# Performance work log

Measured on AMD Instinct MI355X. Metric: run time of the kernel, lower is better.

Reference implementation:

```python
import jax, jax.numpy as jnp
import numpy as np

K = 32  # neighbors per query point


def _gather_points(x, idx):
    # x: [B, N, D], idx: [B, M, k] -> [B, M, k, D]
    B, M, k = idx.shape
    D = x.shape[-1]
    flat = jnp.take_along_axis(x, idx.reshape(B, M * k, 1), axis=1)
    return flat.reshape(B, M, k, D)


def setup_inputs() -> dict:
    key = jax.random.key(0)
    k1, k2, k3, k4, k5 = jax.random.split(key, 5)
    B, N, M, Cin = 16, 4096, 1024, 64
    pos = jax.random.normal(k1, (B, N, 3), dtype=jnp.float32)
    features = jax.random.normal(k2, (B, N, Cin), dtype=jnp.float32)
    idx = jax.random.randint(k3, (B, M), 0, N, dtype=jnp.int64)
    # 1x1 conv2d MLP params: (Cin+3) -> 64 -> 128 (use_xyz adds 3 channels)
    W1 = jax.random.normal(k4, (Cin + 3, 64), dtype=jnp.float32) * (1.0 / np.sqrt(Cin + 3))
    b1 = jnp.zeros((64,), dtype=jnp.float32)
    W2 = jax.random.normal(k5, (64, 128), dtype=jnp.float32) * (1.0 / np.sqrt(64))
    b2 = jnp.zeros((128,), dtype=jnp.float32)
    return {"pos": pos, "features": features, "W1": W1, "b1": b1,
            "W2": W2, "b2": b2, "idx": idx}


def reference(pos, features, W1, b1, W2, b2, idx):
    # pos: [B,N,3], features: [B,N,C], idx: [B,M] query-point indices
    pos_q = jnp.take_along_axis(pos, idx[..., None], axis=1)  # [B,M,3]
    # squared-distance knn: [B,M,N]
    d2 = (jnp.sum(pos_q ** 2, -1, keepdims=True)
          + jnp.sum(pos ** 2, -1)[:, None, :]
          - 2.0 * jnp.einsum("bmd,bnd->bmn", pos_q, pos))
    _, nn_idx = jax.lax.top_k(-d2, K)  # [B,M,K] nearest neighbors
    grouped_pos = _gather_points(pos, nn_idx)          # [B,M,K,3]
    grouped_feat = _gather_points(features, nn_idx)    # [B,M,K,C]
    rel = grouped_pos - pos_q[:, :, None, :]           # recenter groups
    x = jnp.concatenate([rel, grouped_feat], axis=-1)  # [B,M,K,C+3] (use_xyz)
    # 1x1 conv2d MLP == per-point linear + ReLU on channel dim
    h = jax.nn.relu(jnp.einsum("bmkc,cd->bmkd", x, W1) + b1)
    h = jax.nn.relu(jnp.einsum("bmkc,cd->bmkd", h, W2) + b2)
    out = jnp.max(h, axis=-2)  # max over K neighbors -> [B,M,128]
    return (pos_q, out)
```

## Files before the change

### kernel.cpp

```cpp
#include <hip/hip_runtime.h>

#define NPTS  4096
#define MQ    1024
#define BATCH 16
#define KNN   32
#define CIN   64
#define H1D   64
#define H2D   128

typedef _Float16 half8 __attribute__((ext_vector_type(8)));
typedef float    floatx4 __attribute__((ext_vector_type(4)));

#define WS_NN_BYTES ((size_t)BATCH * MQ * KNN * 4)
#define W1F_HALVES  (3 * 4 * 64 * 8)
#define W2F_HALVES  (2 * 8 * 64 * 8)
#define WS_P4_OFF   (WS_NN_BYTES + (W1F_HALVES + W2F_HALVES) * 2)

__global__ __launch_bounds__(256) void wprep_kernel(
    const float* __restrict__ W1, const float* __restrict__ W2,
    const float* __restrict__ pos,
    _Float16* __restrict__ wout, float4* __restrict__ pos4)
{
    const int gid = blockIdx.x * 256 + threadIdx.x;
    if (gid < 768) {
        const int s = gid;
        const int kc = s >> 8, nt = (s >> 6) & 3, lane = s & 63;
        const int col = lane & 15, quad = lane >> 4;
        half8 ph;
#pragma unroll
        for (int j = 0; j < 8; ++j) {
            const int k = kc * 32 + quad * 8 + j;
            ph[j] = (k < 67) ? (_Float16)W1[k * H1D + nt * 16 + col] : (_Float16)0.0f;
        }
        *(half8*)(wout + (size_t)s * 8) = ph;
    } else if (gid < 1792) {
        const int s2 = gid - 768;
        const int kc2 = s2 >> 9, nt2 = (s2 >> 6) & 7, lane = s2 & 63;
        const int col = lane & 15, quad = lane >> 4;
        half8 ph;
#pragma unroll
        for (int j = 0; j < 8; ++j) {
            const int k = kc2 * 32 + quad * 8 + j;
            ph[j] = (_Float16)W2[k * H2D + nt2 * 16 + col];
        }
        *(half8*)(wout + (size_t)W1F_HALVES + (size_t)s2 * 8) = ph;
    } else {
        const int p = gid - 1792;
        if (p < BATCH * NPTS) {
            const float px = pos[p * 3 + 0], py = pos[p * 3 + 1], pz = pos[p * 3 + 2];
            float4 v;
            v.x = px; v.y = py; v.z = pz;
            v.w = __fadd_rn(__fadd_rn(__fmul_rn(px, px), __fmul_rn(py, py)),
                            __fmul_rn(pz, pz));
            pos4[p] = v;
        }
    }
}

__global__ __launch_bounds__(256, 4) void knn_kernel(
    const float4* __restrict__ pos4, const int* __restrict__ idx,
    float* __restrict__ pos_q, int* __restrict__ nn)
{
    const int bid = blockIdx.x;
    const int b   = bid >> 10;
    const int m   = bid & (MQ - 1);
    const int t   = threadIdx.x;
    const int wv  = t >> 6, lane = t & 63;

    __shared__ unsigned int hist[2048];
    __shared__ unsigned int wsum[4];
    __shared__ unsigned int sc[8];
    __shared__ unsigned int ckey[64];
    __shared__ int          cidx[64];
    __shared__ int          outidx[KNN];

    const float4* pb4 = pos4 + (size_t)b * NPTS;
    const int qn = idx[(size_t)b * MQ + m];
    const float4 qv = pb4[qn];
    const float qq = qv.w;

#pragma unroll
    for (int j = 0; j < 8; ++j) hist[t + 256 * j] = 0u;
    __syncthreads();

    float4 p[16];
#pragma unroll
    for (int i = 0; i < 16; ++i) p[i] = pb4[i * 256 + t];

    unsigned int k[16];
#pragma unroll
    for (int i = 0; i < 16; ++i) {
        const float qp = __fadd_rn(__fadd_rn(__fmul_rn(qv.x, p[i].x), __fmul_rn(qv.y, p[i].y)),
                                   __fmul_rn(qv.z, p[i].z));
        const float d2 = __fsub_rn(__fadd_rn(qq, p[i].w), __fmul_rn(2.0f, qp));
        unsigned int u = __float_as_uint(d2);
        u = (u & 0x80000000u) ? ~u : (u | 0x80000000u);
        k[i] = u;
        atomicAdd(&hist[u >> 21], 1u);
    }
    __syncthreads();

    unsigned int prefix = 0u, rank = KNN - 1;
    int shift = 21, bcnt;
    for (int level = 0; level < 3; ++level) {
        const int nb = (level < 2) ? 11 : 10;
        const int g  = (1 << nb) >> 8;
        unsigned int cnt[8];
        unsigned int s = 0;
        for (int j = 0; j < g; ++j) { cnt[j] = hist[t * g + j]; s += cnt[j]; }
        unsigned int v = s;
#pragma unroll
        for (int off = 1; off < 64; off <<= 1) {
            const unsigned int o = __shfl_up(v, off);
            if (lane >= off) v += o;
        }
        if (lane == 63) wsum[wv] = v;
        __syncthreads();
        unsigned int woff = 0;
        for (int i = 0; i < wv; ++i) woff += wsum[i];
        const unsigned int incl = woff + v, excl = incl - s;
        if (rank >= excl && rank < incl) {
            unsigned int e = excl;
            for (int j = 0; j < g; ++j) {
                if (rank < e + cnt[j]) {
                    sc[0] = (prefix << nb) | (unsigned int)(t * g + j);
                    sc[1] = rank - e;
                    sc[2] = cnt[j];
                    break;
                }
                e += cnt[j];
            }
        }
        __syncthreads();
        prefix = sc[0];
        rank   = sc[1];
        bcnt   = (int)sc[2];
        if (level == 2 || bcnt <= 64) break;

        const int nshift = (level == 0) ? 10 : 0;
        const int nnb    = (level == 0) ? 11 : 10;
        const unsigned int nmask = (1u << nnb) - 1u;
        __syncthreads();
#pragma unroll
        for (int j = 0; j < 8; ++j) hist[t + 256 * j] = 0u;
        __syncthreads();
#pragma unroll
        for (int i = 0; i < 16; ++i) {
            const unsigned int u = k[i];
            if ((u >> (nshift + nnb)) == prefix)
                atomicAdd(&hist[(u >> nshift) & nmask], 1u);
        }
        shift = nshift;
        __syncthreads();
    }

    if (t == 0) { sc[3] = 0u; sc[4] = 0u; }
    __syncthreads();
#pragma unroll
    for (int i = 0; i < 16; ++i) {
        const unsigned int u = k[i];
        const unsigned int hp = (shift == 0) ? u : (u >> shift);
        if (hp < prefix) {
            outidx[atomicAdd(&sc[3], 1u)] = i * 256 + t;
        } else if (hp == prefix) {
            const unsigned int slot = atomicAdd(&sc[4], 1u);
            if (slot < 64u) { ckey[slot] = u; cidx[slot] = i * 256 + t; }
        }
    }
    __syncthreads();
    const int defcnt  = (int)sc[3];
    const int candcnt = min((int)sc[4], 64);

    if (wv == 0) {
        const unsigned int k_l = (lane < candcnt) ? ckey[lane] : 0xFFFFFFFFu;
        const int          i_l = (lane < candcnt) ? cidx[lane] : 0x7FFFFFFF;
        int rk = 0;
        for (int j = 0; j < candcnt; ++j) {
            const unsigned int kj = __shfl(k_l, j);
            const int          ij = __shfl(i_l, j);
            if (kj < k_l || (kj == k_l && ij < i_l)) ++rk;
        }
        if (lane < candcnt && rk <= (int)rank) outidx[defcnt + rk] = i_l;
    }
    __syncthreads();
    if (t < KNN) nn[(size_t)bid * KNN + t] = outidx[t];
    if (t == 0) {
        pos_q[(size_t)bid * 3 + 0] = qv.x;
        pos_q[(size_t)bid * 3 + 1] = qv.y;
        pos_q[(size_t)bid * 3 + 2] = qv.z;
    }
}

__global__ __launch_bounds__(256, 4) void mlp_kernel(
    const float4* __restrict__ pos4, const float* __restrict__ feat,
    const float* __restrict__ b1, const float* __restrict__ b2,
    const float* __restrict__ pos_q, const int* __restrict__ nn,
    const _Float16* __restrict__ wf, float* __restrict__ out)
{
    __shared__ _Float16 sh[4 * 3072];
    const int t = threadIdx.x;
    const int w = t >> 6, lane = t & 63;
    const int col = lane & 15, quad = lane >> 4;
    const int q = blockIdx.x * 4 + w;
    const int b = q >> 10;
    const int wbase = w * 3072;

    {
        const int r = t >> 1, h = t & 1;
        const int kk = r & 31;
        const int n = nn[(size_t)q * KNN + kk];
        const float4 pv = pos4[(size_t)b * NPTS + n];
        const float4* f4 = (const float4*)(feat + ((size_t)b * NPTS + n) * CIN);
        const int mt = kk >> 4, lrow = kk & 15;
        if (h == 0) {
            float4 ff[12];
#pragma unroll
            for (int ii = 0; ii < 12; ++ii) ff[ii] = f4[ii];
            float rel[3];
            rel[0] = pv.x - pos_q[(size_t)q * 3 + 0];
            rel[1] = pv.y - pos_q[(size_t)q * 3 + 1];
            rel[2] = pv.z - pos_q[(size_t)q * 3 + 2];
#pragma unroll
            for (int ci = 0; ci < 6; ++ci) {
                half8 ph;
#pragma unroll
                for (int jj = 0; jj < 8; ++jj) {
                    const int c = ci * 8 + jj;
                    float v;
                    if (c < 3) v = rel[c];
                    else {
                        const int fc = c - 3;
                        const float4 vv = ff[fc >> 2];
                        v = ((fc & 3) == 0) ? vv.x : ((fc & 3) == 1) ? vv.y
                          : ((fc & 3) == 2) ? vv.z : vv.w;
                    }
                    ph[jj] = (_Float16)v;
                }
                const int kc = ci >> 2, qd = ci & 3;
                *(half8*)&sh[wbase + ((kc * 2 + mt) * 64 + qd * 16 + lrow) * 8] = ph;
            }
        } else {
            float4 ff[5];
#pragma unroll
            for (int ii = 0; ii < 5; ++ii) ff[ii] = f4[11 + ii];
#pragma unroll
            for (int ci = 6; ci < 12; ++ci) {
                half8 ph;
#pragma unroll
                for (int jj = 0; jj < 8; ++jj) {
                    const int c = ci * 8 + jj;
                    float v = 0.0f;
                    if (c < 67) {
                        const int fc = c - 3;
                        const float4 vv = ff[(fc >> 2) - 11];
                        v = ((fc & 3) == 0) ? vv.x : ((fc & 3) == 1) ? vv.y
                          : ((fc & 3) == 2) ? vv.z : vv.w;
                    }
                    ph[jj] = (_Float16)v;
                }
                const int kc = ci >> 2, qd = ci & 3;
                *(half8*)&sh[wbase + ((kc * 2 + mt) * 64 + qd * 16 + lrow) * 8] = ph;
            }
        }
    }

    half8 af[3][2];
#pragma unroll
    for (int kc = 0; kc < 3; ++kc)
#pragma unroll
        for (int mt = 0; mt < 2; ++mt)
            af[kc][mt] = *(const half8*)&sh[wbase + ((kc * 2 + mt) * 64 + lane) * 8];

    half8 w1f[3][4];
#pragma unroll
    for (int kc = 0; kc < 3; ++kc)
#pragma unroll
        for (int nt = 0; nt < 4; ++nt)
            w1f[kc][nt] = *(const half8*)(wf + (size_t)((kc * 4 + nt) * 64 + lane) * 8);

#pragma unroll
    for (int nt = 0; nt < 4; ++nt) {
        const float bv = b1[nt * 16 + col];
        floatx4 acc0 = {bv, bv, bv, bv}, acc1 = acc0;
#pragma unroll
        for (int kc = 0; kc < 3; ++kc) {
            acc0 = __builtin_amdgcn_mfma_f32_16x16x32_f16(af[kc][0], w1f[kc][nt], acc0, 0, 0, 0);
            acc1 = __builtin_amdgcn_mfma_f32_16x16x32_f16(af[kc][1], w1f[kc][nt], acc1, 0, 0, 0);
        }
        const int kc2 = nt >> 1;
        const int quad2 = (((nt & 1) * 16) + col) >> 3;
        const int j2 = col & 7;
#pragma unroll
        for (int mt = 0; mt < 2; ++mt) {
            const floatx4 a = mt ? acc1 : acc0;
#pragma unroll
            for (int reg = 0; reg < 4; ++reg) {
                const int row = quad * 4 + reg;
                sh[wbase + ((kc2 * 2 + mt) * 64 + quad2 * 16 + row) * 8 + j2] =
                    (_Float16)fmaxf(a[reg], 0.0f);
            }
        }
    }

    half8 a2[2][2];
#pragma unroll
    for (int kc2 = 0; kc2 < 2; ++kc2)
#pragma unroll
        for (int mt = 0; mt < 2; ++mt)
            a2[kc2][mt] = *(const half8*)&sh[wbase + ((kc2 * 2 + mt) * 64 + lane) * 8];

    half8 w2f[2][8];
#pragma unroll
    for (int kc2 = 0; kc2 < 2; ++kc2)
#pragma unroll
        for (int nt2 = 0; nt2 < 8; ++nt2)
            w2f[kc2][nt2] = *(const half8*)(wf + (size_t)W1F_HALVES
                                            + (size_t)((kc2 * 8 + nt2) * 64 + lane) * 8);

    float* oq = out + (size_t)q * H2D;
#pragma unroll
    for (int nt2 = 0; nt2 < 8; ++nt2) {
        const float bv = b2[nt2 * 16 + col];
        floatx4 acc0 = {bv, bv, bv, bv}, acc1 = acc0;
#pragma unroll
        for (int kc2 = 0; kc2 < 2; ++kc2) {
            acc0 = __builtin_amdgcn_mfma_f32_16x16x32_f16(a2[kc2][0], w2f[kc2][nt2], acc0, 0, 0, 0);
            acc1 = __builtin_amdgcn_mfma_f32_16x16x32_f16(a2[kc2][1], w2f[kc2][nt2], acc1, 0, 0, 0);
        }
        float mm = fmaxf(fmaxf(fmaxf(acc0[0], acc0[1]), fmaxf(acc0[2], acc0[3])),
                         fmaxf(fmaxf(acc1[0], acc1[1]), fmaxf(acc1[2], acc1[3])));
        mm = fmaxf(mm, 0.0f);
        mm = fmaxf(mm, __shfl_xor(mm, 16));
        mm = fmaxf(mm, __shfl_xor(mm, 32));
        if (lane < 16) oq[nt2 * 16 + lane] = mm;
    }
}

extern "C" void kernel_launch(void* const* d_in, const int* in_sizes, int n_in,
                              void* d_out, int out_size, void* d_ws, size_t ws_size,
                              hipStream_t stream)
{
    const float* pos  = (const float*)d_in[0];
    const float* feat = (const float*)d_in[1];
    const float* W1   = (const float*)d_in[2];
    const float* b1   = (const float*)d_in[3];
    const float* W2   = (const float*)d_in[4];
    const float* b2   = (const float*)d_in[5];
    const int*   idx  = (const int*)d_in[6];

    float* pos_q = (float*)d_out;
    float* out   = (float*)d_out + (size_t)BATCH * MQ * 3;
    int*      nn = (int*)d_ws;
    _Float16* wf = (_Float16*)((char*)d_ws + WS_NN_BYTES);
    float4*   p4 = (float4*)((char*)d_ws + WS_P4_OFF);

    const int prep_threads = 1792 + BATCH * NPTS;
    wprep_kernel<<<(prep_threads + 255) / 256, 256, 0, stream>>>(W1, W2, pos, wf, p4);
    knn_kernel<<<BATCH * MQ, 256, 0, stream>>>(p4, idx, pos_q, nn);
    mlp_kernel<<<BATCH * MQ / 4, 256, 0, stream>>>(p4, feat, b1, b2,
                                                   pos_q, nn, wf, out);
}
```

Baseline: 196.7 us.

## Use data-adaptive range-normalized radix select in KNN kernel

The KNN radix selection now does a block-wide min/max reduction of the distance keys, subtracts the minimum, and builds 1024-bin histograms over only the occupied bit range. The fixed 11/11/10-bit scheme wasted most of its first-level bins on the sign and exponent bits. The aim is to cut histogram passes and shrink shared-memory histogram work, with vectorized uint4 clears and reads. The cost is an extra reduction and barrier, and a possibly different number of refinement levels.

```diff
diff --git a/kernel.cpp b/kernel.cpp
--- a/kernel.cpp
+++ b/kernel.cpp
@@ -67,7 +67,8 @@
     const int t   = threadIdx.x;
     const int wv  = t >> 6, lane = t & 63;
 
-    __shared__ unsigned int hist[2048];
+    __shared__ __align__(16) unsigned int hist[1024];
+    __shared__ unsigned int wred[8];
     __shared__ unsigned int wsum[4];
     __shared__ unsigned int sc[8];
     __shared__ unsigned int ckey[64];
@@ -79,15 +80,14 @@
     const float4 qv = pb4[qn];
     const float qq = qv.w;
 
-#pragma unroll
-    for (int j = 0; j < 8; ++j) hist[t + 256 * j] = 0u;
-    __syncthreads();
+    *(uint4*)&hist[t * 4] = make_uint4(0u, 0u, 0u, 0u);
 
     float4 p[16];
 #pragma unroll
     for (int i = 0; i < 16; ++i) p[i] = pb4[i * 256 + t];
 
     unsigned int k[16];
+    unsigned int lmin = 0xFFFFFFFFu, lmax = 0u;
 #pragma unroll
     for (int i = 0; i < 16; ++i) {
         const float qp = __fadd_rn(__fadd_rn(__fmul_rn(qv.x, p[i].x), __fmul_rn(qv.y, p[i].y)),
@@ -96,19 +96,39 @@
         unsigned int u = __float_as_uint(d2);
         u = (u & 0x80000000u) ? ~u : (u | 0x80000000u);
         k[i] = u;
-        atomicAdd(&hist[u >> 21], 1u);
-    }
+        lmin = min(lmin, u);
+        lmax = max(lmax, u);
+    }
+#pragma unroll
+    for (int off = 32; off; off >>= 1) {
+        lmin = min(lmin, (unsigned int)__shfl_xor(lmin, off));
+        lmax = max(lmax, (unsigned int)__shfl_xor(lmax, off));
+    }
+    if (lane == 0) { wred[wv] = lmin; wred[4 + wv] = lmax; }
+    __syncthreads();
+    const unsigned int umin = min(min(wred[0], wred[1]), min(wred[2], wred[3]));
+    const unsigned int umax = max(max(wred[4], wred[5]), max(wred[6], wred[7]));
+    const unsigned int rng  = umax - umin;
+#pragma unroll
+    for (int i = 0; i < 16; ++i) k[i] -= umin;
+
+    int sCur;
+    {
+        const int bits = (rng == 0u) ? 0 : (32 - __clz(rng));
+        sCur = (bits > 10) ? (bits - 10) : 0;
+    }
+
+#pragma unroll
+    for (int i = 0; i < 16; ++i) atomicAdd(&hist[k[i] >> sCur], 1u);
     __syncthreads();
 
     unsigned int prefix = 0u, rank = KNN - 1;
-    int shift = 21, bcnt;
-    for (int level = 0; level < 3; ++level) {
-        const int nb = (level < 2) ? 11 : 10;
-        const int g  = (1 << nb) >> 8;
-        unsigned int cnt[8];
-        unsigned int s = 0;
-        for (int j = 0; j < g; ++j) { cnt[j] = hist[t * g + j]; s += cnt[j]; }
-        unsigned int v = s;
+    int bcnt = 0, nb = 0;
+    bool first = true;
+    for (;;) {
+        const uint4 c4 = *(const uint4*)&hist[t * 4];
+        const unsigned int ssum = c4.x + c4.y + c4.z + c4.w;
+        unsigned int v = ssum;
 #pragma unroll
         for (int off = 1; off < 64; off <<= 1) {
             const unsigned int o = __shfl_up(v, off);
@@ -118,12 +138,13 @@
         __syncthreads();
         unsigned int woff = 0;
         for (int i = 0; i < wv; ++i) woff += wsum[i];
-        const unsigned int incl = woff + v, excl = incl - s;
+        const unsigned int incl = woff + v, excl = incl - ssum;
         if (rank >= excl && rank < incl) {
+            const unsigned int cnt[4] = {c4.x, c4.y, c4.z, c4.w};
             unsigned int e = excl;
-            for (int j = 0; j < g; ++j) {
+            for (int j = 0; j < 4; ++j) {
                 if (rank < e + cnt[j]) {
-                    sc[0] = (prefix << nb) | (unsigned int)(t * g + j);
+                    sc[0] = (unsigned int)(t * 4 + j);
                     sc[1] = rank - e;
                     sc[2] = cnt[j];
                     break;
@@ -132,39 +153,38 @@
             }
         }
         __syncthreads();
-        prefix = sc[0];
-        rank   = sc[1];
-        bcnt   = (int)sc[2];
-        if (level == 2 || bcnt <= 64) break;
-
-        const int nshift = (level == 0) ? 10 : 0;
-        const int nnb    = (level == 0) ? 11 : 10;
-        const unsigned int nmask = (1u << nnb) - 1u;
-        __syncthreads();
-#pragma unroll
-        for (int j = 0; j < 8; ++j) hist[t + 256 * j] = 0u;
-        __syncthreads();
+        const unsigned int bin = sc[0];
+        rank = sc[1];
+        bcnt = (int)sc[2];
+        prefix = first ? bin : ((prefix << nb) | bin);
+        first = false;
+        if (bcnt <= 64 || sCur == 0) break;
+
+        const int sNext = (sCur > 10) ? (sCur - 10) : 0;
+        nb = sCur - sNext;
+        __syncthreads();
+        *(uint4*)&hist[t * 4] = make_uint4(0u, 0u, 0u, 0u);
+        __syncthreads();
+        const unsigned int mask = (1u << nb) - 1u;
 #pragma unroll
         for (int i = 0; i < 16; ++i) {
-            const unsigned int u = k[i];
-            if ((u >> (nshift + nnb)) == prefix)
-                atomicAdd(&hist[(u >> nshift) & nmask], 1u);
-        }
-        shift = nshift;
-        __syncthreads();
+            if ((k[i] >> sCur) == prefix)
+                atomicAdd(&hist[(k[i] >> sNext) & mask], 1u);
+        }
+        __syncthreads();
+        sCur = sNext;
     }
 
     if (t == 0) { sc[3] = 0u; sc[4] = 0u; }
     __syncthreads();
 #pragma unroll
     for (int i = 0; i < 16; ++i) {
-        const unsigned int u = k[i];
-        const unsigned int hp = (shift == 0) ? u : (u >> shift);
+        const unsigned int hp = k[i] >> sCur;
         if (hp < prefix) {
             outidx[atomicAdd(&sc[3], 1u)] = i * 256 + t;
         } else if (hp == prefix) {
             const unsigned int slot = atomicAdd(&sc[4], 1u);
-            if (slot < 64u) { ckey[slot] = u; cidx[slot] = i * 256 + t; }
+            if (slot < 64u) { ckey[slot] = k[i]; cidx[slot] = i * 256 + t; }
         }
     }
     __syncthreads();
```

New measurement: 190.4 us. 3.2% less time.

## Replace radix-histogram kNN select with group-min threshold filter and rank sort

Applied to the files above, without the earlier changes.

Replaces the multi-level radix histogram selection in the kNN kernel with a threshold computed as the 32nd smallest of 64 per-group minima, which is an upper bound on the 32nd-nearest distance. Points at or below the threshold are compacted into shared memory and ranked by an O(n^2) pairwise count, with a slow 32-round argmin fallback if more than 512 candidates survive. This removes the histogram clears, shared atomics and repeated scans, at the cost of a candidate count that depends on the data and possible extra work in the fallback path.

```diff
diff --git a/kernel.cpp b/kernel.cpp
--- a/kernel.cpp
+++ b/kernel.cpp
@@ -61,33 +61,31 @@
     const float4* __restrict__ pos4, const int* __restrict__ idx,
     float* __restrict__ pos_q, int* __restrict__ nn)
 {
+    const int KCAP = 512;
     const int bid = blockIdx.x;
     const int b   = bid >> 10;
     const int m   = bid & (MQ - 1);
     const int t   = threadIdx.x;
     const int wv  = t >> 6, lane = t & 63;
 
-    __shared__ unsigned int hist[2048];
-    __shared__ unsigned int wsum[4];
-    __shared__ unsigned int sc[8];
-    __shared__ unsigned int ckey[64];
-    __shared__ int          cidx[64];
-    __shared__ int          outidx[KNN];
+    __shared__ unsigned int gmin[64];
+    __shared__ uint2 cand[512];
+    __shared__ unsigned int sc[2];
+    __shared__ unsigned long long w64[4];
 
     const float4* pb4 = pos4 + (size_t)b * NPTS;
     const int qn = idx[(size_t)b * MQ + m];
     const float4 qv = pb4[qn];
     const float qq = qv.w;
 
-#pragma unroll
-    for (int j = 0; j < 8; ++j) hist[t + 256 * j] = 0u;
-    __syncthreads();
+    if (t == 0) sc[1] = 0u;
 
     float4 p[16];
 #pragma unroll
     for (int i = 0; i < 16; ++i) p[i] = pb4[i * 256 + t];
 
     unsigned int k[16];
+    unsigned int lmin = 0xFFFFFFFFu;
 #pragma unroll
     for (int i = 0; i < 16; ++i) {
         const float qp = __fadd_rn(__fadd_rn(__fmul_rn(qv.x, p[i].x), __fmul_rn(qv.y, p[i].y)),
@@ -96,94 +94,76 @@
         unsigned int u = __float_as_uint(d2);
         u = (u & 0x80000000u) ? ~u : (u | 0x80000000u);
         k[i] = u;
-        atomicAdd(&hist[u >> 21], 1u);
-    }
+        lmin = min(lmin, u);
+    }
+
+    lmin = min(lmin, (unsigned int)__shfl_xor((int)lmin, 1));
+    lmin = min(lmin, (unsigned int)__shfl_xor((int)lmin, 2));
+    if ((lane & 3) == 0) gmin[t >> 2] = lmin;
     __syncthreads();
 
-    unsigned int prefix = 0u, rank = KNN - 1;
-    int shift = 21, bcnt;
-    for (int level = 0; level < 3; ++level) {
-        const int nb = (level < 2) ? 11 : 10;
-        const int g  = (1 << nb) >> 8;
-        unsigned int cnt[8];
-        unsigned int s = 0;
-        for (int j = 0; j < g; ++j) { cnt[j] = hist[t * g + j]; s += cnt[j]; }
-        unsigned int v = s;
-#pragma unroll
-        for (int off = 1; off < 64; off <<= 1) {
-            const unsigned int o = __shfl_up(v, off);
-            if (lane >= off) v += o;
-        }
-        if (lane == 63) wsum[wv] = v;
-        __syncthreads();
-        unsigned int woff = 0;
-        for (int i = 0; i < wv; ++i) woff += wsum[i];
-        const unsigned int incl = woff + v, excl = incl - s;
-        if (rank >= excl && rank < incl) {
-            unsigned int e = excl;
-            for (int j = 0; j < g; ++j) {
-                if (rank < e + cnt[j]) {
-                    sc[0] = (prefix << nb) | (unsigned int)(t * g + j);
-                    sc[1] = rank - e;
-                    sc[2] = cnt[j];
-                    break;
-                }
-                e += cnt[j];
-            }
-        }
-        __syncthreads();
-        prefix = sc[0];
-        rank   = sc[1];
-        bcnt   = (int)sc[2];
-        if (level == 2 || bcnt <= 64) break;
-
-        const int nshift = (level == 0) ? 10 : 0;
-        const int nnb    = (level == 0) ? 11 : 10;
-        const unsigned int nmask = (1u << nnb) - 1u;
-        __syncthreads();
-#pragma unroll
-        for (int j = 0; j < 8; ++j) hist[t + 256 * j] = 0u;
-        __syncthreads();
-#pragma unroll
-        for (int i = 0; i < 16; ++i) {
-            const unsigned int u = k[i];
-            if ((u >> (nshift + nnb)) == prefix)
-                atomicAdd(&hist[(u >> nshift) & nmask], 1u);
-        }
-        shift = nshift;
-        __syncthreads();
-    }
-
-    if (t == 0) { sc[3] = 0u; sc[4] = 0u; }
+    if (wv == 0) {
+        const unsigned int g = gmin[lane];
+        int rk = 0;
+        for (int j = 0; j < 64; ++j) {
+            const unsigned int gj = (unsigned int)__shfl((int)g, j);
+            if (gj < g || (gj == g && j < lane)) ++rk;
+        }
+        if (rk == 31) sc[0] = g;
+    }
     __syncthreads();
+    const unsigned int T = sc[0];
+
 #pragma unroll
     for (int i = 0; i < 16; ++i) {
-        const unsigned int u = k[i];
-        const unsigned int hp = (shift == 0) ? u : (u >> shift);
-        if (hp < prefix) {
-            outidx[atomicAdd(&sc[3], 1u)] = i * 256 + t;
-        } else if (hp == prefix) {
-            const unsigned int slot = atomicAdd(&sc[4], 1u);
-            if (slot < 64u) { ckey[slot] = u; cidx[slot] = i * 256 + t; }
+        if (k[i] <= T) {
+            const unsigned int slot = atomicAdd(&sc[1], 1u);
+            if (slot < (unsigned)KCAP)
+                cand[slot] = make_uint2(k[i], (unsigned int)(i * 256 + t));
         }
     }
     __syncthreads();
-    const int defcnt  = (int)sc[3];
-    const int candcnt = min((int)sc[4], 64);
-
-    if (wv == 0) {
-        const unsigned int k_l = (lane < candcnt) ? ckey[lane] : 0xFFFFFFFFu;
-        const int          i_l = (lane < candcnt) ? cidx[lane] : 0x7FFFFFFF;
-        int rk = 0;
-        for (int j = 0; j < candcnt; ++j) {
-            const unsigned int kj = __shfl(k_l, j);
-            const int          ij = __shfl(i_l, j);
-            if (kj < k_l || (kj == k_l && ij < i_l)) ++rk;
-        }
-        if (lane < candcnt && rk <= (int)rank) outidx[defcnt + rk] = i_l;
-    }
-    __syncthreads();
-    if (t < KNN) nn[(size_t)bid * KNN + t] = outidx[t];
+    const int candcnt = (int)sc[1];
+
+    if (candcnt <= KCAP) {
+        if (t < candcnt) {
+            const uint2 my = cand[t];
+            int rk = 0;
+            for (int j = 0; j < candcnt; ++j) {
+                const uint2 c = cand[j];
+                if (c.x < my.x || (c.x == my.x && c.y < my.y)) ++rk;
+            }
+            if (rk < KNN) nn[(size_t)bid * KNN + rk] = (int)my.y;
+        }
+    } else {
+        unsigned long long last = 0ull;
+        for (int r = 0; r < KNN; ++r) {
+            __syncthreads();
+            unsigned long long best = ~0ull;
+#pragma unroll
+            for (int i = 0; i < 16; ++i) {
+                const unsigned long long pk =
+                    ((unsigned long long)k[i] << 32) | (unsigned int)(i * 256 + t);
+                if ((r == 0 || pk > last) && pk < best) best = pk;
+            }
+#pragma unroll
+            for (int off = 1; off < 64; off <<= 1) {
+                const unsigned long long o = __shfl_xor(best, off);
+                if (o < best) best = o;
+            }
+            if (lane == 0) w64[wv] = best;
+            __syncthreads();
+            if (t == 0) {
+                unsigned long long bb = w64[0];
+                for (int wi = 1; wi < 4; ++wi) if (w64[wi] < bb) bb = w64[wi];
+                w64[0] = bb;
+                nn[(size_t)bid * KNN + r] = (int)(bb & 0xFFFFFFFFu);
+            }
+            __syncthreads();
+            last = w64[0];
+        }
+    }
+
     if (t == 0) {
         pos_q[(size_t)bid * 3 + 0] = qv.x;
         pos_q[(size_t)bid * 3 + 1] = qv.y;
```

Measured after the change: 208.1 us. 1.06x slower.
